# Kernel tuning notes

Hardware: AMD Instinct MI355X
Metric: run time of the kernel (lower is better)

## Reference

```python
import jax, jax.numpy as jnp
import numpy as np

DIM = 768
NUM_HEADS = 12
LATENT_LEN = 32


def setup_inputs() -> dict:
    key = jax.random.key(0)
    k1, k2, k3, k4 = jax.random.split(key, 4)
    x = jax.random.normal(k1, (32, 4096, DIM), dtype=jnp.float32)
    latent = jax.random.normal(k2, (1, LATENT_LEN, DIM), dtype=jnp.float32) * 0.02
    # torch nn.Linear(dim, dim): weight [out, in], bias [out]
    bound = 1.0 / np.sqrt(DIM)
    v_w = jax.random.uniform(k3, (DIM, DIM), dtype=jnp.float32, minval=-bound, maxval=bound)
    v_b = jax.random.uniform(k4, (DIM,), dtype=jnp.float32, minval=-bound, maxval=bound)
    return {"x": x, "latent": latent, "v_w": v_w, "v_b": v_b}


def reference(x, latent, v_w, v_b):
    B, N, C = x.shape
    H = NUM_HEADS
    hd = C // H
    L = LATENT_LEN
    chunk = C // L
    scale = hd ** (-0.5)

    # q: [L, H, hd] from latent (shared across batch)
    q = latent[0].reshape(L, H, hd)
    # k: [B, N, H, hd]
    k = x.reshape(B, N, H, hd)
    # attn logits: [B, H, L, N]
    attn = jnp.einsum("lhd,bnhd->bhln", q * scale, k)
    attn = jax.nn.softmax(attn, axis=-1)
    attn = attn.mean(axis=1)  # [B, L, N] (head-mean before value matmul)

    # v: Linear then split channels by latent_len -> [B, L, N, chunk]
    v = (jnp.einsum("bnc,dc->bnd", x, v_w) + v_b).reshape(B, N, L, chunk)
    out = jnp.einsum("bln,blnc->blc", attn, v.transpose(0, 2, 1, 3))
    return out.reshape(B, 1, C)
```

## Files before the change

kernel.cpp:

```cpp
#include <hip/hip_runtime.h>
#include <cstdint>


typedef short bf16x8 __attribute__((ext_vector_type(8)));
typedef float f32x4 __attribute__((ext_vector_type(4)));

#define MFMA16(a, b, c) __builtin_amdgcn_mfma_f32_16x16x32_bf16((a), (b), (c), 0, 0, 0)

__device__ __forceinline__ uint32_t pk_bf16(float a, float b) {
    return __builtin_amdgcn_perm(__float_as_uint(b), __float_as_uint(a), 0x07060302u);
}
__device__ __forceinline__ unsigned short bf16_trunc(float f) {
    return (unsigned short)(__float_as_uint(f) >> 16);
}
__device__ __forceinline__ float bf16_lo(uint32_t u) { return __uint_as_float(u << 16); }
__device__ __forceinline__ float bf16_hi(uint32_t u) { return __uint_as_float(u & 0xffff0000u); }

__global__ __launch_bounds__(256)
void k1_logits(const float* __restrict__ x, const float* __restrict__ latent,
               unsigned short* __restrict__ E)
{
    const int b   = blockIdx.x >> 6;
    const int n0  = (blockIdx.x & 63) << 6;
    const int tid = threadIdx.x;
    const int wv  = tid >> 6;
    const int lane = tid & 63;
    const int quad = lane >> 4;
    const int lc   = lane & 15;

    __shared__ unsigned short q_lds[32][72];
    __shared__ unsigned short x_lds[64][72];

    const int n = n0 + wv * 16 + lc;

    for (int h = 0; h < 12; ++h) {
        __syncthreads();
        for (int i = tid; i < 512; i += 256) {
            int l = i >> 4, f4 = i & 15;
            float4 qv = *(const float4*)&latent[l * 768 + h * 64 + f4 * 4];
            uint2 p;
            p.x = pk_bf16(qv.x * 0.125f, qv.y * 0.125f);
            p.y = pk_bf16(qv.z * 0.125f, qv.w * 0.125f);
            *(uint2*)&q_lds[l][f4 * 4] = p;
        }
        for (int i = tid; i < 1024; i += 256) {
            int nn = i >> 4, f4 = i & 15;
            float4 xv = *(const float4*)&x[(b * 4096 + n0 + nn) * 768 + h * 64 + f4 * 4];
            uint2 p;
            p.x = pk_bf16(xv.x, xv.y);
            p.y = pk_bf16(xv.z, xv.w);
            *(uint2*)&x_lds[nn][f4 * 4] = p;
        }
        __syncthreads();

        bf16x8 a00 = *(const bf16x8*)&q_lds[lc][quad * 8];
        bf16x8 a01 = *(const bf16x8*)&q_lds[lc][32 + quad * 8];
        bf16x8 a10 = *(const bf16x8*)&q_lds[16 + lc][quad * 8];
        bf16x8 a11 = *(const bf16x8*)&q_lds[16 + lc][32 + quad * 8];
        bf16x8 b0  = *(const bf16x8*)&x_lds[wv * 16 + lc][quad * 8];
        bf16x8 b1  = *(const bf16x8*)&x_lds[wv * 16 + lc][32 + quad * 8];

        f32x4 c0 = {0.f, 0.f, 0.f, 0.f};
        f32x4 c1 = {0.f, 0.f, 0.f, 0.f};
        c0 = MFMA16(a00, b0, c0);
        c0 = MFMA16(a01, b1, c0);
        c1 = MFMA16(a10, b0, c1);
        c1 = MFMA16(a11, b1, c1);

        unsigned short* Eh = E + (size_t)((b * 12 + h) * 32) * 4096;
        #pragma unroll
        for (int r = 0; r < 4; ++r) {
            Eh[(quad * 4 + r) * 4096 + n]      = bf16_trunc(__expf(c0[r]));
            Eh[(16 + quad * 4 + r) * 4096 + n] = bf16_trunc(__expf(c1[r]));
        }
    }
}

__global__ __launch_bounds__(256)
void kw_weights(const unsigned short* __restrict__ E, unsigned short* __restrict__ W)
{
    const int b = blockIdx.x >> 5;
    const int l = blockIdx.x & 31;
    const int tid = threadIdx.x;
    const int wv = tid >> 6, lane = tid & 63;

    const unsigned short* Eb = E + (size_t)(b * 384 + l) * 4096;
    __shared__ float red[12][4];
    __shared__ float rsl[12];

    float s[12];
    #pragma unroll
    for (int h = 0; h < 12; ++h) {
        const uint4* p = (const uint4*)(Eb + (size_t)h * 131072 + tid * 16);
        uint4 u0 = p[0], u1 = p[1];
        float v = 0.f;
        v += bf16_lo(u0.x) + bf16_hi(u0.x) + bf16_lo(u0.y) + bf16_hi(u0.y);
        v += bf16_lo(u0.z) + bf16_hi(u0.z) + bf16_lo(u0.w) + bf16_hi(u0.w);
        v += bf16_lo(u1.x) + bf16_hi(u1.x) + bf16_lo(u1.y) + bf16_hi(u1.y);
        v += bf16_lo(u1.z) + bf16_hi(u1.z) + bf16_lo(u1.w) + bf16_hi(u1.w);
        #pragma unroll
        for (int m = 1; m < 64; m <<= 1) v += __shfl_xor(v, m);
        s[h] = v;
    }
    if (lane == 0) {
        #pragma unroll
        for (int h = 0; h < 12; ++h) red[h][wv] = s[h];
    }
    __syncthreads();
    if (tid < 12) rsl[tid] = 1.0f / (12.0f * (red[tid][0] + red[tid][1] + red[tid][2] + red[tid][3]));
    __syncthreads();

    float acc[16];
    #pragma unroll
    for (int i = 0; i < 16; ++i) acc[i] = 0.f;
    #pragma unroll
    for (int h = 0; h < 12; ++h) {
        float r = rsl[h];
        const uint4* p = (const uint4*)(Eb + (size_t)h * 131072 + tid * 16);
        uint4 u0 = p[0], u1 = p[1];
        acc[0] += bf16_lo(u0.x) * r;  acc[1] += bf16_hi(u0.x) * r;
        acc[2] += bf16_lo(u0.y) * r;  acc[3] += bf16_hi(u0.y) * r;
        acc[4] += bf16_lo(u0.z) * r;  acc[5] += bf16_hi(u0.z) * r;
        acc[6] += bf16_lo(u0.w) * r;  acc[7] += bf16_hi(u0.w) * r;
        acc[8] += bf16_lo(u1.x) * r;  acc[9] += bf16_hi(u1.x) * r;
        acc[10] += bf16_lo(u1.y) * r; acc[11] += bf16_hi(u1.y) * r;
        acc[12] += bf16_lo(u1.z) * r; acc[13] += bf16_hi(u1.z) * r;
        acc[14] += bf16_lo(u1.w) * r; acc[15] += bf16_hi(u1.w) * r;
    }
    uint4 o0, o1;
    o0.x = pk_bf16(acc[0], acc[1]);   o0.y = pk_bf16(acc[2], acc[3]);
    o0.z = pk_bf16(acc[4], acc[5]);   o0.w = pk_bf16(acc[6], acc[7]);
    o1.x = pk_bf16(acc[8], acc[9]);   o1.y = pk_bf16(acc[10], acc[11]);
    o1.z = pk_bf16(acc[12], acc[13]); o1.w = pk_bf16(acc[14], acc[15]);
    uint4* wp = (uint4*)(W + (size_t)(b * 32 + l) * 4096 + tid * 16);
    wp[0] = o0; wp[1] = o1;
}

__global__ __launch_bounds__(64)
void yacc_kernel(const float* __restrict__ x, const unsigned short* __restrict__ W,
                 float* __restrict__ yws)
{
    const int bx  = blockIdx.x;
    const int b   = bx / 96;
    const int rem = bx - b * 96;
    const int ct  = rem % 12;
    const int g   = rem / 12;
    const int lane = threadIdx.x;
    const int quad = lane >> 4;
    const int lc   = lane & 15;
    const int c0   = ct * 64;
    const int nb   = g * 512;

    const float* xb = x + (size_t)b * 4096 * 768;
    const unsigned short* Wb = W + (size_t)b * 32 * 4096;

    f32x4 acc[2][4];
    #pragma unroll
    for (int t = 0; t < 2; ++t)
        #pragma unroll
        for (int s = 0; s < 4; ++s) acc[t][s] = (f32x4){0.f, 0.f, 0.f, 0.f};

    for (int kk = 0; kk < 512; kk += 32) {
        const int n = nb + kk + quad * 8;
        bf16x8 a0 = *(const bf16x8*)&Wb[lc * 4096 + n];
        bf16x8 a1 = *(const bf16x8*)&Wb[(16 + lc) * 4096 + n];
        #pragma unroll
        for (int s = 0; s < 4; ++s) {
            const float* xp = xb + (size_t)n * 768 + c0 + s * 16 + lc;
            float f0 = xp[0], f1 = xp[768], f2 = xp[1536], f3 = xp[2304];
            float f4 = xp[3072], f5 = xp[3840], f6 = xp[4608], f7 = xp[5376];
            union { uint32_t u[4]; bf16x8 v; } bb;
            bb.u[0] = pk_bf16(f0, f1);
            bb.u[1] = pk_bf16(f2, f3);
            bb.u[2] = pk_bf16(f4, f5);
            bb.u[3] = pk_bf16(f6, f7);
            acc[0][s] = MFMA16(a0, bb.v, acc[0][s]);
            acc[1][s] = MFMA16(a1, bb.v, acc[1][s]);
        }
    }

    float* yp = yws + (size_t)((g * 32 + b) * 32) * 768;
    #pragma unroll
    for (int t = 0; t < 2; ++t)
        #pragma unroll
        for (int s = 0; s < 4; ++s)
            #pragma unroll
            for (int r = 0; r < 4; ++r)
                yp[(t * 16 + quad * 4 + r) * 768 + c0 + s * 16 + lc] = acc[t][s][r];
}

__global__ __launch_bounds__(256)
void out_kernel(const float* __restrict__ yws, const float* __restrict__ vw,
                const float* __restrict__ vb, float* __restrict__ out)
{
    const int b = blockIdx.x >> 5;
    const int l = blockIdx.x & 31;
    const int tid = threadIdx.x;
    __shared__ float y_lds[768];
    for (int c = tid; c < 768; c += 256) {
        float v = 0.f;
        #pragma unroll
        for (int g = 0; g < 8; ++g)
            v += yws[(size_t)((g * 32 + b) * 32 + l) * 768 + c];
        y_lds[c] = v;
    }
    __syncthreads();
    const int wv = tid >> 6, lane = tid & 63;
    for (int i = wv; i < 24; i += 4) {
        const int row = l * 24 + i;
        const float* wr = vw + row * 768;
        float p = 0.f;
        #pragma unroll
        for (int j = 0; j < 12; ++j)
            p += y_lds[j * 64 + lane] * wr[j * 64 + lane];
        #pragma unroll
        for (int m = 1; m < 64; m <<= 1) p += __shfl_xor(p, m);
        if (lane == 0) out[b * 768 + row] = p + vb[row];
    }
}

extern "C" void kernel_launch(void* const* d_in, const int* in_sizes, int n_in,
                              void* d_out, int out_size, void* d_ws, size_t ws_size,
                              hipStream_t stream)
{
    const float* x      = (const float*)d_in[0];
    const float* latent = (const float*)d_in[1];
    const float* vw     = (const float*)d_in[2];
    const float* vb     = (const float*)d_in[3];
    float* out = (float*)d_out;

    char* ws = (char*)d_ws;
    unsigned short* E   = (unsigned short*)ws;
    unsigned short* W   = (unsigned short*)(ws + 100663296);
    float*          yws = (float*)(ws + 109051904);

    k1_logits<<<dim3(2048), dim3(256), 0, stream>>>(x, latent, E);
    kw_weights<<<dim3(1024), dim3(256), 0, stream>>>(E, W);
    yacc_kernel<<<dim3(3072), dim3(64), 0, stream>>>(x, W, yws);
    out_kernel<<<dim3(1024), dim3(256), 0, stream>>>(yws, vw, vb, out);
}
```

Baseline: 689.6 us.

## Load logits operands directly into registers, widen weight kernel, split yacc finer

The logits kernel drops its shared-memory staging and the two barriers per head. Each lane now loads its x and latent fragments straight from global memory into MFMA operands, and the 1/8 scale moves to the exp argument. The weight-averaging kernel runs 512 threads that each hold 8 elements, caching the loaded E values in registers so the second pass does not reload them. The yacc kernel splits N into 16 groups instead of 8 to get more blocks, and the output kernel reduces over 16 partials, which adds more partial-sum traffic.

```diff
diff --git a/kernel.cpp b/kernel.cpp
--- a/kernel.cpp
+++ b/kernel.cpp
@@ -16,67 +16,69 @@
 __device__ __forceinline__ float bf16_lo(uint32_t u) { return __uint_as_float(u << 16); }
 __device__ __forceinline__ float bf16_hi(uint32_t u) { return __uint_as_float(u & 0xffff0000u); }
 
+__device__ __forceinline__ bf16x8 pack8(float4 a, float4 b) {
+    union { uint32_t u[4]; bf16x8 v; } r;
+    r.u[0] = pk_bf16(a.x, a.y); r.u[1] = pk_bf16(a.z, a.w);
+    r.u[2] = pk_bf16(b.x, b.y); r.u[3] = pk_bf16(b.z, b.w);
+    return r.v;
+}
+
 __global__ __launch_bounds__(256)
-void k1_logits(const float* __restrict__ x, const float* __restrict__ latent,
+void ka_logits(const float* __restrict__ x, const float* __restrict__ latent,
                unsigned short* __restrict__ E)
 {
-    const int b   = blockIdx.x >> 6;
-    const int n0  = (blockIdx.x & 63) << 6;
-    const int tid = threadIdx.x;
-    const int wv  = tid >> 6;
-    const int lane = tid & 63;
+    const int b  = blockIdx.x >> 6;
+    const int n0 = (blockIdx.x & 63) << 6;
+    const int wv = threadIdx.x >> 6;
+    const int lane = threadIdx.x & 63;
     const int quad = lane >> 4;
     const int lc   = lane & 15;
-
-    __shared__ unsigned short q_lds[32][72];
-    __shared__ unsigned short x_lds[64][72];
-
     const int n = n0 + wv * 16 + lc;
 
+    const float* xr = x + (size_t)(b * 4096 + n) * 768;
+    const float* q0 = latent + lc * 768;
+    const float* q1 = latent + (16 + lc) * 768;
+
     for (int h = 0; h < 12; ++h) {
-        __syncthreads();
-        for (int i = tid; i < 512; i += 256) {
-            int l = i >> 4, f4 = i & 15;
-            float4 qv = *(const float4*)&latent[l * 768 + h * 64 + f4 * 4];
-            uint2 p;
-            p.x = pk_bf16(qv.x * 0.125f, qv.y * 0.125f);
-            p.y = pk_bf16(qv.z * 0.125f, qv.w * 0.125f);
-            *(uint2*)&q_lds[l][f4 * 4] = p;
-        }
-        for (int i = tid; i < 1024; i += 256) {
-            int nn = i >> 4, f4 = i & 15;
-            float4 xv = *(const float4*)&x[(b * 4096 + n0 + nn) * 768 + h * 64 + f4 * 4];
-            uint2 p;
-            p.x = pk_bf16(xv.x, xv.y);
-            p.y = pk_bf16(xv.z, xv.w);
-            *(uint2*)&x_lds[nn][f4 * 4] = p;
-        }
-        __syncthreads();
-
-        bf16x8 a00 = *(const bf16x8*)&q_lds[lc][quad * 8];
-        bf16x8 a01 = *(const bf16x8*)&q_lds[lc][32 + quad * 8];
-        bf16x8 a10 = *(const bf16x8*)&q_lds[16 + lc][quad * 8];
-        bf16x8 a11 = *(const bf16x8*)&q_lds[16 + lc][32 + quad * 8];
-        bf16x8 b0  = *(const bf16x8*)&x_lds[wv * 16 + lc][quad * 8];
-        bf16x8 b1  = *(const bf16x8*)&x_lds[wv * 16 + lc][32 + quad * 8];
+        const int d0 = h * 64 + quad * 8;
+
+        float4 x0a = *(const float4*)(xr + d0);
+        float4 x0b = *(const float4*)(xr + d0 + 4);
+        float4 x1a = *(const float4*)(xr + d0 + 32);
+        float4 x1b = *(const float4*)(xr + d0 + 36);
+        float4 p0a = *(const float4*)(q0 + d0);
+        float4 p0b = *(const float4*)(q0 + d0 + 4);
+        float4 p1a = *(const float4*)(q0 + d0 + 32);
+        float4 p1b = *(const float4*)(q0 + d0 + 36);
+        float4 r0a = *(const float4*)(q1 + d0);
+        float4 r0b = *(const float4*)(q1 + d0 + 4);
+        float4 r1a = *(const float4*)(q1 + d0 + 32);
+        float4 r1b = *(const float4*)(q1 + d0 + 36);
+
+        bf16x8 bf0 = pack8(x0a, x0b);
+        bf16x8 bf1 = pack8(x1a, x1b);
+        bf16x8 a00 = pack8(p0a, p0b);
+        bf16x8 a01 = pack8(p1a, p1b);
+        bf16x8 a10 = pack8(r0a, r0b);
+        bf16x8 a11 = pack8(r1a, r1b);
 
         f32x4 c0 = {0.f, 0.f, 0.f, 0.f};
         f32x4 c1 = {0.f, 0.f, 0.f, 0.f};
-        c0 = MFMA16(a00, b0, c0);
-        c0 = MFMA16(a01, b1, c0);
-        c1 = MFMA16(a10, b0, c1);
-        c1 = MFMA16(a11, b1, c1);
+        c0 = MFMA16(a00, bf0, c0);
+        c0 = MFMA16(a01, bf1, c0);
+        c1 = MFMA16(a10, bf0, c1);
+        c1 = MFMA16(a11, bf1, c1);
 
         unsigned short* Eh = E + (size_t)((b * 12 + h) * 32) * 4096;
         #pragma unroll
         for (int r = 0; r < 4; ++r) {
-            Eh[(quad * 4 + r) * 4096 + n]      = bf16_trunc(__expf(c0[r]));
-            Eh[(16 + quad * 4 + r) * 4096 + n] = bf16_trunc(__expf(c1[r]));
+            Eh[(quad * 4 + r) * 4096 + n]      = bf16_trunc(__expf(c0[r] * 0.125f));
+            Eh[(16 + quad * 4 + r) * 4096 + n] = bf16_trunc(__expf(c1[r] * 0.125f));
         }
     }
 }
 
-__global__ __launch_bounds__(256)
+__global__ __launch_bounds__(512)
 void kw_weights(const unsigned short* __restrict__ E, unsigned short* __restrict__ W)
 {
     const int b = blockIdx.x >> 5;
@@ -85,55 +87,49 @@
     const int wv = tid >> 6, lane = tid & 63;
 
     const unsigned short* Eb = E + (size_t)(b * 384 + l) * 4096;
-    __shared__ float red[12][4];
-    __shared__ float rsl[12];
-
+
+    uint4 u[12];
     float s[12];
     #pragma unroll
     for (int h = 0; h < 12; ++h) {
-        const uint4* p = (const uint4*)(Eb + (size_t)h * 131072 + tid * 16);
-        uint4 u0 = p[0], u1 = p[1];
-        float v = 0.f;
-        v += bf16_lo(u0.x) + bf16_hi(u0.x) + bf16_lo(u0.y) + bf16_hi(u0.y);
-        v += bf16_lo(u0.z) + bf16_hi(u0.z) + bf16_lo(u0.w) + bf16_hi(u0.w);
-        v += bf16_lo(u1.x) + bf16_hi(u1.x) + bf16_lo(u1.y) + bf16_hi(u1.y);
-        v += bf16_lo(u1.z) + bf16_hi(u1.z) + bf16_lo(u1.w) + bf16_hi(u1.w);
+        u[h] = *(const uint4*)(Eb + (size_t)h * 131072 + tid * 8);
+        float v = bf16_lo(u[h].x) + bf16_hi(u[h].x) + bf16_lo(u[h].y) + bf16_hi(u[h].y)
+                + bf16_lo(u[h].z) + bf16_hi(u[h].z) + bf16_lo(u[h].w) + bf16_hi(u[h].w);
         #pragma unroll
         for (int m = 1; m < 64; m <<= 1) v += __shfl_xor(v, m);
         s[h] = v;
     }
+
+    __shared__ float red[12][8];
+    __shared__ float rsl[12];
     if (lane == 0) {
         #pragma unroll
         for (int h = 0; h < 12; ++h) red[h][wv] = s[h];
     }
     __syncthreads();
-    if (tid < 12) rsl[tid] = 1.0f / (12.0f * (red[tid][0] + red[tid][1] + red[tid][2] + red[tid][3]));
+    if (tid < 12) {
+        float t = 0.f;
+        #pragma unroll
+        for (int w = 0; w < 8; ++w) t += red[tid][w];
+        rsl[tid] = 1.0f / (12.0f * t);
+    }
     __syncthreads();
 
-    float acc[16];
-    #pragma unroll
-    for (int i = 0; i < 16; ++i) acc[i] = 0.f;
+    float acc[8];
+    #pragma unroll
+    for (int i = 0; i < 8; ++i) acc[i] = 0.f;
     #pragma unroll
     for (int h = 0; h < 12; ++h) {
         float r = rsl[h];
-        const uint4* p = (const uint4*)(Eb + (size_t)h * 131072 + tid * 16);
-        uint4 u0 = p[0], u1 = p[1];
-        acc[0] += bf16_lo(u0.x) * r;  acc[1] += bf16_hi(u0.x) * r;
-        acc[2] += bf16_lo(u0.y) * r;  acc[3] += bf16_hi(u0.y) * r;
-        acc[4] += bf16_lo(u0.z) * r;  acc[5] += bf16_hi(u0.z) * r;
-        acc[6] += bf16_lo(u0.w) * r;  acc[7] += bf16_hi(u0.w) * r;
-        acc[8] += bf16_lo(u1.x) * r;  acc[9] += bf16_hi(u1.x) * r;
-        acc[10] += bf16_lo(u1.y) * r; acc[11] += bf16_hi(u1.y) * r;
-        acc[12] += bf16_lo(u1.z) * r; acc[13] += bf16_hi(u1.z) * r;
-        acc[14] += bf16_lo(u1.w) * r; acc[15] += bf16_hi(u1.w) * r;
-    }
-    uint4 o0, o1;
-    o0.x = pk_bf16(acc[0], acc[1]);   o0.y = pk_bf16(acc[2], acc[3]);
-    o0.z = pk_bf16(acc[4], acc[5]);   o0.w = pk_bf16(acc[6], acc[7]);
-    o1.x = pk_bf16(acc[8], acc[9]);   o1.y = pk_bf16(acc[10], acc[11]);
-    o1.z = pk_bf16(acc[12], acc[13]); o1.w = pk_bf16(acc[14], acc[15]);
-    uint4* wp = (uint4*)(W + (size_t)(b * 32 + l) * 4096 + tid * 16);
-    wp[0] = o0; wp[1] = o1;
+        acc[0] += bf16_lo(u[h].x) * r;  acc[1] += bf16_hi(u[h].x) * r;
+        acc[2] += bf16_lo(u[h].y) * r;  acc[3] += bf16_hi(u[h].y) * r;
+        acc[4] += bf16_lo(u[h].z) * r;  acc[5] += bf16_hi(u[h].z) * r;
+        acc[6] += bf16_lo(u[h].w) * r;  acc[7] += bf16_hi(u[h].w) * r;
+    }
+    uint4 o;
+    o.x = pk_bf16(acc[0], acc[1]); o.y = pk_bf16(acc[2], acc[3]);
+    o.z = pk_bf16(acc[4], acc[5]); o.w = pk_bf16(acc[6], acc[7]);
+    *(uint4*)(W + (size_t)(b * 32 + l) * 4096 + tid * 8) = o;
 }
 
 __global__ __launch_bounds__(64)
@@ -141,15 +137,15 @@
                  float* __restrict__ yws)
 {
     const int bx  = blockIdx.x;
-    const int b   = bx / 96;
-    const int rem = bx - b * 96;
+    const int b   = bx / 192;
+    const int rem = bx - b * 192;
     const int ct  = rem % 12;
     const int g   = rem / 12;
     const int lane = threadIdx.x;
     const int quad = lane >> 4;
     const int lc   = lane & 15;
     const int c0   = ct * 64;
-    const int nb   = g * 512;
+    const int nb   = g * 256;
 
     const float* xb = x + (size_t)b * 4096 * 768;
     const unsigned short* Wb = W + (size_t)b * 32 * 4096;
@@ -160,7 +156,7 @@
         #pragma unroll
         for (int s = 0; s < 4; ++s) acc[t][s] = (f32x4){0.f, 0.f, 0.f, 0.f};
 
-    for (int kk = 0; kk < 512; kk += 32) {
+    for (int kk = 0; kk < 256; kk += 32) {
         const int n = nb + kk + quad * 8;
         bf16x8 a0 = *(const bf16x8*)&Wb[lc * 4096 + n];
         bf16x8 a1 = *(const bf16x8*)&Wb[(16 + lc) * 4096 + n];
@@ -200,7 +196,7 @@
     for (int c = tid; c < 768; c += 256) {
         float v = 0.f;
         #pragma unroll
-        for (int g = 0; g < 8; ++g)
+        for (int g = 0; g < 16; ++g)
             v += yws[(size_t)((g * 32 + b) * 32 + l) * 768 + c];
         y_lds[c] = v;
     }
@@ -234,8 +230,8 @@
     unsigned short* W   = (unsigned short*)(ws + 100663296);
     float*          yws = (float*)(ws + 109051904);
 
-    k1_logits<<<dim3(2048), dim3(256), 0, stream>>>(x, latent, E);
-    kw_weights<<<dim3(1024), dim3(256), 0, stream>>>(E, W);
-    yacc_kernel<<<dim3(3072), dim3(64), 0, stream>>>(x, W, yws);
+    ka_logits<<<dim3(2048), dim3(256), 0, stream>>>(x, latent, E);
+    kw_weights<<<dim3(1024), dim3(512), 0, stream>>>(E, W);
+    yacc_kernel<<<dim3(6144), dim3(64), 0, stream>>>(x, W, yws);
     out_kernel<<<dim3(1024), dim3(256), 0, stream>>>(yws, vw, vb, out);
 }
```

New measurement: 744.9 us. 8.0% more time.
